# Kernel optimization log

Measured on AMD Instinct MI355X. Metric: run time of the kernel, lower is better.

Reference implementation:

```python
import jax, jax.numpy as jnp
import numpy as np

B, T, D = 2048, 60, 6
H, F, O = 64, 10, 1


def setup_inputs() -> dict:
    key = jax.random.key(0)
    ks = jax.random.split(key, 16)
    w = lambda k, shape, s=0.1: jax.random.normal(k, shape, jnp.float32) * s
    return {
        "x": jax.random.normal(ks[0], (B, T, D), jnp.float32),
        "W_i": w(ks[1], (D, H)), "U_i": w(ks[2], (H, H)), "b_i": jnp.zeros((H,), jnp.float32),
        "W_ste": w(ks[3], (D, H)), "U_ste": w(ks[4], (H, H)), "b_ste": jnp.ones((H,), jnp.float32),
        "W_fre": w(ks[5], (D, F)), "U_fre": w(ks[6], (H, F)), "b_fre": jnp.ones((F,), jnp.float32),
        "W_c": w(ks[7], (D, H)), "U_c": w(ks[8], (H, H)), "b_c": jnp.zeros((H,), jnp.float32),
        "W_o": w(ks[9], (D, H)), "U_o": w(ks[10], (H, H)), "b_o": jnp.zeros((H,), jnp.float32),
        "U_a": w(ks[11], (F, 1)), "b_a": jnp.zeros((H,), jnp.float32),
        "W_p": w(ks[12], (H, O)), "b_p": jnp.zeros((O,), jnp.float32),
    }


def _hsig(v):
    # torch.nn.Hardsigmoid: relu6(x + 3) / 6
    return jnp.clip(v / 6.0 + 0.5, 0.0, 1.0)


def reference(x, W_i, U_i, b_i, W_ste, U_ste, b_ste, W_fre, U_fre, b_fre,
              W_c, U_c, b_c, W_o, U_o, b_o, U_a, b_a, W_p, b_p):
    b, t_len, _ = x.shape
    h_dim = W_i.shape[1]
    f_dim = W_fre.shape[1]
    freq = jnp.arange(f_dim, dtype=x.dtype) / f_dim  # (F,)
    ua = U_a[:, 0]  # (F,)

    def step(carry, x_t):
        h, S_re, S_im, t = carry
        i = _hsig(x_t @ W_i + b_i + h @ U_i)              # (B,H)
        ste = _hsig(x_t @ W_ste + b_ste + h @ U_ste)      # (B,H)
        fre = _hsig(x_t @ W_fre + b_fre + h @ U_fre)      # (B,F)
        f = ste[:, :, None] * fre[:, None, :]             # (B,H,F)
        c = i * jnp.tanh(x_t @ W_c + b_c + h @ U_c)       # (B,H)
        t = t + 1.0
        omega = (2.0 * jnp.pi) * t * freq                  # (F,)
        S_re = f * S_re + c[:, :, None] * jnp.cos(omega)   # (B,H,F)
        S_im = f * S_im + c[:, :, None] * jnp.sin(omega)   # (B,H,F)
        A = S_re * S_re + S_im * S_im                      # (B,H,F)
        a = jnp.tanh(jnp.einsum('bhf,f->bh', A, ua) + b_a)
        o = _hsig(x_t @ W_o + b_o + h @ U_o)
        h = o * a
        return (h, S_re, S_im, t), None

    init = (jnp.zeros((b, h_dim), x.dtype),
            jnp.zeros((b, h_dim, f_dim), x.dtype),
            jnp.zeros((b, h_dim, f_dim), x.dtype),
            jnp.asarray(0.0, x.dtype))
    (h, _, _, _), _ = jax.lax.scan(step, init, jnp.swapaxes(x, 0, 1))
    # original returns p from the last timestep only
    return h @ W_p + b_p
```

## Files before the change

### kernel.cpp

```cpp
#include <hip/hip_runtime.h>


#define BB 2048
#define TT 60
#define DD 6
#define HH 64
#define FF 10
#define NB 4

#define XS 968
#define HS 72

typedef short bf16x8 __attribute__((ext_vector_type(8)));
typedef float f32x4  __attribute__((ext_vector_type(4)));

__device__ __forceinline__ unsigned short f2bf(float f) {
    union { float f; unsigned u; } v; v.f = f;
    unsigned r = v.u + 0x7fffu + ((v.u >> 16) & 1u);
    return (unsigned short)(r >> 16);
}
__device__ __forceinline__ float bf2f(unsigned short b) {
    union { unsigned u; float f; } v; v.u = ((unsigned)b) << 16; return v.f;
}
__device__ __forceinline__ float hsig_f(float v) {
    return fminf(fmaxf(fmaf(v, 0.16666666666666666f, 0.5f), 0.0f), 1.0f);
}
__device__ __forceinline__ float tanh_f(float x) {
    float xc = fminf(fmaxf(x, -12.0f), 12.0f);
    float e  = __builtin_amdgcn_exp2f(xc * 2.8853900817779268f);
    return (e - 1.0f) * __builtin_amdgcn_rcpf(e + 1.0f);
}
__device__ __forceinline__ float uni(float v) {
    return __int_as_float(__builtin_amdgcn_readfirstlane(__float_as_int(v)));
}
__device__ __forceinline__ void pinv(bf16x8& v) { asm volatile("" : "+v"(v)); }

__global__ __launch_bounds__(256, 2)
void sfm_kernel(
    const float* __restrict__ x,
    const float* __restrict__ W_i,  const float* __restrict__ U_i,  const float* __restrict__ b_i,
    const float* __restrict__ W_ste,const float* __restrict__ U_ste,const float* __restrict__ b_ste,
    const float* __restrict__ W_fre,const float* __restrict__ U_fre,const float* __restrict__ b_fre,
    const float* __restrict__ W_c,  const float* __restrict__ U_c,  const float* __restrict__ b_c,
    const float* __restrict__ W_o,  const float* __restrict__ U_o,  const float* __restrict__ b_o,
    const float* __restrict__ U_a,  const float* __restrict__ b_a,
    const float* __restrict__ W_p,  const float* __restrict__ b_p,
    float* __restrict__ out)
{
    const int tid  = threadIdx.x;
    const int lane = tid & 63;
    const int wave = tid >> 6;
    const int q    = lane >> 4;
    const int n16  = lane & 15;
    const int b0   = blockIdx.x * NB;

    __shared__ __align__(16) unsigned short xsp[NB * XS];
    __shared__ __align__(16) unsigned short hhi[NB * HS];
    __shared__ __align__(16) unsigned short hlo[NB * HS];
    __shared__ __align__(16) float zbuf[4 * 64 * NB];
    __shared__ __align__(16) float frebuf[16 * NB];
    __shared__ float red[4][NB];

    for (int item = tid; item < NB * TT; item += 256) {
        const float* xg = x + (size_t)b0 * (TT * DD) + item * DD;
        const int b = item / TT, s = item - b * TT;
        unsigned short* dst = &xsp[b * XS + s * 16];
        #pragma unroll
        for (int d = 0; d < DD; ++d) {
            const float v = xg[d];
            const unsigned short hb = f2bf(v);
            dst[d]     = hb;
            dst[8 + d] = f2bf(v - bf2f(hb));
        }
        dst[6] = 0x3F80; dst[7] = 0;
        dst[14] = 0; dst[15] = 0;
    }
    for (int i = tid; i < NB * HS; i += 256) { hhi[i] = 0; hlo[i] = 0; }

    const float* Ug = (wave == 0) ? U_i : (wave == 1) ? U_ste : (wave == 2) ? U_c : U_o;
    const float* Wg = (wave == 0) ? W_i : (wave == 1) ? W_ste : (wave == 2) ? W_c : W_o;
    const float* bg = (wave == 0) ? b_i : (wave == 1) ? b_ste : (wave == 2) ? b_c : b_o;

    bf16x8 Bh[5][3], Bl[5][3];
    #pragma unroll
    for (int t = 0; t < 5; ++t) {
        #pragma unroll
        for (int c = 0; c < 3; ++c) {
            #pragma unroll
            for (int j = 0; j < 8; ++j) {
                const int kv = c * 32 + q * 8 + j;
                float v = 0.0f;
                if (t < 4) {
                    const int n = t * 16 + n16;
                    if      (kv < 64)  v = Ug[kv * HH + n];
                    else if (kv < 70)  v = Wg[(kv - 64) * HH + n];
                    else if (kv == 70) v = bg[n];
                } else if (wave == 3 && n16 < FF) {
                    if      (kv < 64)  v = U_fre[kv * FF + n16];
                    else if (kv < 70)  v = W_fre[(kv - 64) * FF + n16];
                    else if (kv == 70) v = b_fre[n16];
                }
                const unsigned short hb = f2bf(v);
                Bh[t][c][j] = (short)hb;
                Bl[t][c][j] = (short)f2bf(v - bf2f(hb));
            }
            pinv(Bh[t][c]); pinv(Bl[t][c]);
        }
    }

    const int pb = tid & (NB - 1);
    const int pc = tid >> 2;
    const float bav = b_a[pc];
    const float wpv = W_p[pc];
    const float bpv = uni(b_p[0]);
    float uav[FF];
    #pragma unroll
    for (int f = 0; f < FF; ++f) uav[f] = uni(U_a[f]);

    const float CBt[FF] = { 1.0f,  0.8090169943749475f,  0.30901699437494745f,
                           -0.30901699437494745f, -0.8090169943749475f, -1.0f,
                           -0.8090169943749475f, -0.30901699437494745f,
                            0.30901699437494745f,  0.8090169943749475f };
    const float SBt[FF] = { 0.0f,  0.5877852522924731f,  0.9510565162951535f,
                            0.9510565162951535f,  0.5877852522924731f,  0.0f,
                           -0.5877852522924731f, -0.9510565162951535f,
                           -0.9510565162951535f, -0.5877852522924731f };

    float Sre[FF], Sim[FF], cs[FF], sn[FF];
    #pragma unroll
    for (int f = 0; f < FF; ++f) {
        Sre[f] = 0.0f; Sim[f] = 0.0f; cs[f] = CBt[f]; sn[f] = SBt[f];
    }
    float hv = 0.0f;

    __syncthreads();

    int sm = 0;
    for (int s = 0; s < TT; ++s) {
        const int ab = n16 & (NB - 1);
        bf16x8 Ah[3], Al[3];
        #pragma unroll
        for (int c = 0; c < 2; ++c) {
            Ah[c] = *(const bf16x8*)&hhi[ab * HS + c * 32 + q * 8];
            Al[c] = *(const bf16x8*)&hlo[ab * HS + c * 32 + q * 8];
        }
        {
            const bf16x8 xvh = *(const bf16x8*)&xsp[ab * XS + s * 16];
            const bf16x8 xvl = *(const bf16x8*)&xsp[ab * XS + s * 16 + 8];
            const bf16x8 zf = {0, 0, 0, 0, 0, 0, 0, 0};
            Ah[2] = (q == 0) ? xvh : zf;
            Al[2] = (q == 0) ? xvl : zf;
        }

        f32x4 acc[5];
        #pragma unroll
        for (int t = 0; t < 5; ++t) {
            if (t < 4 || wave == 3) {
                f32x4 a = {0.0f, 0.0f, 0.0f, 0.0f};
                #pragma unroll
                for (int c = 0; c < 3; ++c) {
                    a = __builtin_amdgcn_mfma_f32_16x16x32_bf16(Al[c], Bh[t][c], a, 0, 0, 0);
                    a = __builtin_amdgcn_mfma_f32_16x16x32_bf16(Ah[c], Bl[t][c], a, 0, 0, 0);
                    a = __builtin_amdgcn_mfma_f32_16x16x32_bf16(Ah[c], Bh[t][c], a, 0, 0, 0);
                }
                acc[t] = a;
            }
        }

        if (q == 0) {
            #pragma unroll
            for (int t = 0; t < 4; ++t)
                *(f32x4*)&zbuf[(wave * 64 + t * 16 + n16) * NB] = acc[t];
            if (wave == 3 && n16 < FF)
                *(f32x4*)&frebuf[n16 * NB] = acc[4];
        }
        __syncthreads();

        const float zi = zbuf[(0 * 64 + pc) * NB + pb];
        const float zs = zbuf[(1 * 64 + pc) * NB + pb];
        const float zc = zbuf[(2 * 64 + pc) * NB + pb];
        const float zo = zbuf[(3 * 64 + pc) * NB + pb];
        float fr[FF];
        #pragma unroll
        for (int f = 0; f < FF; ++f) fr[f] = hsig_f(frebuf[f * NB + pb]);

        const float iv  = hsig_f(zi);
        const float stv = hsig_f(zs);
        const float ov  = hsig_f(zo);
        const float cv  = iv * tanh_f(zc);

        if (sm == 0) {
            #pragma unroll
            for (int f = 0; f < FF; ++f) { cs[f] = CBt[f]; sn[f] = SBt[f]; }
        }

        float aacc = bav;
        #pragma unroll
        for (int f = 0; f < FF; ++f) {
            const float fc = stv * fr[f];
            Sre[f] = fmaf(fc, Sre[f], cv * cs[f]);
            Sim[f] = fmaf(fc, Sim[f], cv * sn[f]);
            const float A = fmaf(Sim[f], Sim[f], Sre[f] * Sre[f]);
            aacc = fmaf(A, uav[f], aacc);
            const float cc = cs[f];
            cs[f] = fmaf(cc, CBt[f], -(sn[f] * SBt[f]));
            sn[f] = fmaf(cc, SBt[f],   sn[f] * CBt[f]);
        }
        hv = ov * tanh_f(aacc);

        {
            const unsigned short hb = f2bf(hv);
            hhi[pb * HS + pc] = hb;
            hlo[pb * HS + pc] = f2bf(hv - bf2f(hb));
        }
        if (++sm == 10) sm = 0;
        __syncthreads();
    }

    float val = hv * wpv;
    val += __shfl_xor(val, 4, 64);
    val += __shfl_xor(val, 8, 64);
    val += __shfl_xor(val, 16, 64);
    val += __shfl_xor(val, 32, 64);
    if (lane < NB) red[wave][lane] = val;
    __syncthreads();
    if (tid < NB)
        out[b0 + tid] = red[0][tid] + red[1][tid] + red[2][tid] + red[3][tid] + bpv;
}

extern "C" void kernel_launch(void* const* d_in, const int* in_sizes, int n_in,
                              void* d_out, int out_size, void* d_ws, size_t ws_size,
                              hipStream_t stream) {
    (void)in_sizes; (void)n_in; (void)d_ws; (void)ws_size; (void)out_size;
    const float* x     = (const float*)d_in[0];
    const float* W_i   = (const float*)d_in[1];
    const float* U_i   = (const float*)d_in[2];
    const float* b_i   = (const float*)d_in[3];
    const float* W_ste = (const float*)d_in[4];
    const float* U_ste = (const float*)d_in[5];
    const float* b_ste = (const float*)d_in[6];
    const float* W_fre = (const float*)d_in[7];
    const float* U_fre = (const float*)d_in[8];
    const float* b_fre = (const float*)d_in[9];
    const float* W_c   = (const float*)d_in[10];
    const float* U_c   = (const float*)d_in[11];
    const float* b_c   = (const float*)d_in[12];
    const float* W_o   = (const float*)d_in[13];
    const float* U_o   = (const float*)d_in[14];
    const float* b_o   = (const float*)d_in[15];
    const float* U_a   = (const float*)d_in[16];
    const float* b_a   = (const float*)d_in[17];
    const float* W_p   = (const float*)d_in[18];
    const float* b_p   = (const float*)d_in[19];

    sfm_kernel<<<BB / NB, 256, 0, stream>>>(
        x, W_i, U_i, b_i, W_ste, U_ste, b_ste, W_fre, U_fre, b_fre,
        W_c, U_c, b_c, W_o, U_o, b_o, U_a, b_a, W_p, b_p, (float*)d_out);
}
```

Measured before the change: 177.3 us.

## Unroll recurrence by period 10 to make twiddles compile-time constants and interleave MFMAs

The time loop is split into 6 outer iterations of 10 fully unrolled steps. Because omega has period 10, the cos/sin twiddle factors become compile-time constants indexed by (f*(k+1))%10, which removes the per-step rotation recurrence and the reset branch. The five MFMA accumulation chains are also interleaved so independent accumulators overlap instead of running serially, and hardsigmoid uses a single med3 instruction. The full unroll grows code size and may raise register pressure.

```diff
diff --git a/kernel.cpp b/kernel.cpp
--- a/kernel.cpp
+++ b/kernel.cpp
@@ -23,7 +23,7 @@
     union { unsigned u; float f; } v; v.u = ((unsigned)b) << 16; return v.f;
 }
 __device__ __forceinline__ float hsig_f(float v) {
-    return fminf(fmaxf(fmaf(v, 0.16666666666666666f, 0.5f), 0.0f), 1.0f);
+    return __builtin_amdgcn_fmed3f(fmaf(v, 0.16666666666666666f, 0.5f), 0.0f, 1.0f);
 }
 __device__ __forceinline__ float tanh_f(float x) {
     float xc = fminf(fmaxf(x, -12.0f), 12.0f);
@@ -117,104 +117,101 @@
     #pragma unroll
     for (int f = 0; f < FF; ++f) uav[f] = uni(U_a[f]);
 
-    const float CBt[FF] = { 1.0f,  0.8090169943749475f,  0.30901699437494745f,
-                           -0.30901699437494745f, -0.8090169943749475f, -1.0f,
-                           -0.8090169943749475f, -0.30901699437494745f,
-                            0.30901699437494745f,  0.8090169943749475f };
-    const float SBt[FF] = { 0.0f,  0.5877852522924731f,  0.9510565162951535f,
-                            0.9510565162951535f,  0.5877852522924731f,  0.0f,
-                           -0.5877852522924731f, -0.9510565162951535f,
-                           -0.9510565162951535f, -0.5877852522924731f };
-
-    float Sre[FF], Sim[FF], cs[FF], sn[FF];
+    const float CT[FF] = { 1.0f,  0.8090169943749475f,  0.30901699437494745f,
+                          -0.30901699437494745f, -0.8090169943749475f, -1.0f,
+                          -0.8090169943749475f, -0.30901699437494745f,
+                           0.30901699437494745f,  0.8090169943749475f };
+    const float ST[FF] = { 0.0f,  0.5877852522924731f,  0.9510565162951535f,
+                           0.9510565162951535f,  0.5877852522924731f,  0.0f,
+                          -0.5877852522924731f, -0.9510565162951535f,
+                          -0.9510565162951535f, -0.5877852522924731f };
+
+    float Sre[FF], Sim[FF];
     #pragma unroll
-    for (int f = 0; f < FF; ++f) {
-        Sre[f] = 0.0f; Sim[f] = 0.0f; cs[f] = CBt[f]; sn[f] = SBt[f];
-    }
+    for (int f = 0; f < FF; ++f) { Sre[f] = 0.0f; Sim[f] = 0.0f; }
     float hv = 0.0f;
 
+    const int ab = n16 & (NB - 1);
+    const unsigned short* hhp = &hhi[ab * HS];
+    const unsigned short* hlp = &hlo[ab * HS];
+
     __syncthreads();
 
-    int sm = 0;
-    for (int s = 0; s < TT; ++s) {
-        const int ab = n16 & (NB - 1);
-        bf16x8 Ah[3], Al[3];
+    for (int sQ = 0; sQ < 6; ++sQ) {
+        const unsigned short* xrow = &xsp[ab * XS + sQ * 160];
         #pragma unroll
-        for (int c = 0; c < 2; ++c) {
-            Ah[c] = *(const bf16x8*)&hhi[ab * HS + c * 32 + q * 8];
-            Al[c] = *(const bf16x8*)&hlo[ab * HS + c * 32 + q * 8];
+        for (int k = 0; k < 10; ++k) {
+            bf16x8 Ah[3], Al[3];
+            #pragma unroll
+            for (int c = 0; c < 2; ++c) {
+                Ah[c] = *(const bf16x8*)&hhp[c * 32 + q * 8];
+                Al[c] = *(const bf16x8*)&hlp[c * 32 + q * 8];
+            }
+            {
+                const bf16x8 xvh = *(const bf16x8*)&xrow[k * 16];
+                const bf16x8 xvl = *(const bf16x8*)&xrow[k * 16 + 8];
+                const bf16x8 zf = {0, 0, 0, 0, 0, 0, 0, 0};
+                Ah[2] = (q == 0) ? xvh : zf;
+                Al[2] = (q == 0) ? xvl : zf;
+            }
+
+            f32x4 acc0 = {0.f,0.f,0.f,0.f}, acc1 = acc0, acc2 = acc0, acc3 = acc0, acc4 = acc0;
+            #pragma unroll
+            for (int c = 0; c < 3; ++c) {
+                #pragma unroll
+                for (int tm = 0; tm < 3; ++tm) {
+                    const bf16x8 a = (tm == 0) ? Al[c] : Ah[c];
+                    acc0 = __builtin_amdgcn_mfma_f32_16x16x32_bf16(a, (tm==1) ? Bl[0][c] : Bh[0][c], acc0, 0, 0, 0);
+                    acc1 = __builtin_amdgcn_mfma_f32_16x16x32_bf16(a, (tm==1) ? Bl[1][c] : Bh[1][c], acc1, 0, 0, 0);
+                    acc2 = __builtin_amdgcn_mfma_f32_16x16x32_bf16(a, (tm==1) ? Bl[2][c] : Bh[2][c], acc2, 0, 0, 0);
+                    acc3 = __builtin_amdgcn_mfma_f32_16x16x32_bf16(a, (tm==1) ? Bl[3][c] : Bh[3][c], acc3, 0, 0, 0);
+                    if (wave == 3)
+                        acc4 = __builtin_amdgcn_mfma_f32_16x16x32_bf16(a, (tm==1) ? Bl[4][c] : Bh[4][c], acc4, 0, 0, 0);
+                }
+            }
+
+            if (q == 0) {
+                *(f32x4*)&zbuf[(wave * 64 +  0 + n16) * NB] = acc0;
+                *(f32x4*)&zbuf[(wave * 64 + 16 + n16) * NB] = acc1;
+                *(f32x4*)&zbuf[(wave * 64 + 32 + n16) * NB] = acc2;
+                *(f32x4*)&zbuf[(wave * 64 + 48 + n16) * NB] = acc3;
+                if (wave == 3 && n16 < FF)
+                    *(f32x4*)&frebuf[n16 * NB] = acc4;
+            }
+            __syncthreads();
+
+            const float zi = zbuf[(0 * 64 + pc) * NB + pb];
+            const float zs = zbuf[(1 * 64 + pc) * NB + pb];
+            const float zc = zbuf[(2 * 64 + pc) * NB + pb];
+            const float zo = zbuf[(3 * 64 + pc) * NB + pb];
+            float fr[FF];
+            #pragma unroll
+            for (int f = 0; f < FF; ++f) fr[f] = hsig_f(frebuf[f * NB + pb]);
+
+            const float iv  = hsig_f(zi);
+            const float stv = hsig_f(zs);
+            const float ov  = hsig_f(zo);
+            const float cv  = iv * tanh_f(zc);
+
+            float aacc = bav;
+            #pragma unroll
+            for (int f = 0; f < FF; ++f) {
+                const int idx = (f * ((k + 1) % 10)) % 10;
+                const float fc = stv * fr[f];
+                Sre[f] = fmaf(fc, Sre[f], cv * CT[idx]);
+                Sim[f] = fmaf(fc, Sim[f], cv * ST[idx]);
+                const float A = fmaf(Sim[f], Sim[f], Sre[f] * Sre[f]);
+                aacc = fmaf(A, uav[f], aacc);
+            }
+            hv = ov * tanh_f(aacc);
+
+            {
+                const unsigned short hb = f2bf(hv);
+                hhi[pb * HS + pc] = hb;
+                hlo[pb * HS + pc] = f2bf(hv - bf2f(hb));
+            }
+            __syncthreads();
         }
-        {
-            const bf16x8 xvh = *(const bf16x8*)&xsp[ab * XS + s * 16];
-            const bf16x8 xvl = *(const bf16x8*)&xsp[ab * XS + s * 16 + 8];
-            const bf16x8 zf = {0, 0, 0, 0, 0, 0, 0, 0};
-            Ah[2] = (q == 0) ? xvh : zf;
-            Al[2] = (q == 0) ? xvl : zf;
-        }
-
-        f32x4 acc[5];
-        #pragma unroll
-        for (int t = 0; t < 5; ++t) {
-            if (t < 4 || wave == 3) {
-                f32x4 a = {0.0f, 0.0f, 0.0f, 0.0f};
-                #pragma unroll
-                for (int c = 0; c < 3; ++c) {
-                    a = __builtin_amdgcn_mfma_f32_16x16x32_bf16(Al[c], Bh[t][c], a, 0, 0, 0);
-                    a = __builtin_amdgcn_mfma_f32_16x16x32_bf16(Ah[c], Bl[t][c], a, 0, 0, 0);
-                    a = __builtin_amdgcn_mfma_f32_16x16x32_bf16(Ah[c], Bh[t][c], a, 0, 0, 0);
-                }
-                acc[t] = a;
-            }
-        }
-
-        if (q == 0) {
-            #pragma unroll
-            for (int t = 0; t < 4; ++t)
-                *(f32x4*)&zbuf[(wave * 64 + t * 16 + n16) * NB] = acc[t];
-            if (wave == 3 && n16 < FF)
-                *(f32x4*)&frebuf[n16 * NB] = acc[4];
-        }
-        __syncthreads();
-
-        const float zi = zbuf[(0 * 64 + pc) * NB + pb];
-        const float zs = zbuf[(1 * 64 + pc) * NB + pb];
-        const float zc = zbuf[(2 * 64 + pc) * NB + pb];
-        const float zo = zbuf[(3 * 64 + pc) * NB + pb];
-        float fr[FF];
-        #pragma unroll
-        for (int f = 0; f < FF; ++f) fr[f] = hsig_f(frebuf[f * NB + pb]);
-
-        const float iv  = hsig_f(zi);
-        const float stv = hsig_f(zs);
-        const float ov  = hsig_f(zo);
-        const float cv  = iv * tanh_f(zc);
-
-        if (sm == 0) {
-            #pragma unroll
-            for (int f = 0; f < FF; ++f) { cs[f] = CBt[f]; sn[f] = SBt[f]; }
-        }
-
-        float aacc = bav;
-        #pragma unroll
-        for (int f = 0; f < FF; ++f) {
-            const float fc = stv * fr[f];
-            Sre[f] = fmaf(fc, Sre[f], cv * cs[f]);
-            Sim[f] = fmaf(fc, Sim[f], cv * sn[f]);
-            const float A = fmaf(Sim[f], Sim[f], Sre[f] * Sre[f]);
-            aacc = fmaf(A, uav[f], aacc);
-            const float cc = cs[f];
-            cs[f] = fmaf(cc, CBt[f], -(sn[f] * SBt[f]));
-            sn[f] = fmaf(cc, SBt[f],   sn[f] * CBt[f]);
-        }
-        hv = ov * tanh_f(aacc);
-
-        {
-            const unsigned short hb = f2bf(hv);
-            hhi[pb * HS + pc] = hb;
-            hlo[pb * HS + pc] = f2bf(hv - bf2f(hb));
-        }
-        if (++sm == 10) sm = 0;
-        __syncthreads();
     }
 
     float val = hv * wpv;
```

Result: faster. 166.8 us (-5.9%).

## Double batch per block and split gate columns across eight waves

Applied to the files above, without the earlier changes.

Each block now handles 8 batch rows with 512 threads. Each of the 8 waves computes half the columns of one gate (2 MFMA tiles instead of 4), and the frequency gate moves to wave 7. Batch rows now fill 8 of the 16 MFMA M rows, so less of each matrix op is wasted, and each wave has a shorter serial MFMA chain per step. The MFMA loop is also interleaved across accumulators for ILP, and hardsigmoid uses fmed3. The cost is half as many blocks and larger blocks that may limit occupancy.

```diff
diff --git a/kernel.cpp b/kernel.cpp
--- a/kernel.cpp
+++ b/kernel.cpp
@@ -6,7 +6,7 @@
 #define DD 6
 #define HH 64
 #define FF 10
-#define NB 4
+#define NB 8
 
 #define XS 968
 #define HS 72
@@ -23,7 +23,7 @@
     union { unsigned u; float f; } v; v.u = ((unsigned)b) << 16; return v.f;
 }
 __device__ __forceinline__ float hsig_f(float v) {
-    return fminf(fmaxf(fmaf(v, 0.16666666666666666f, 0.5f), 0.0f), 1.0f);
+    return __builtin_amdgcn_fmed3f(fmaf(v, 0.16666666666666666f, 0.5f), 0.0f, 1.0f);
 }
 __device__ __forceinline__ float tanh_f(float x) {
     float xc = fminf(fmaxf(x, -12.0f), 12.0f);
@@ -35,7 +35,7 @@
 }
 __device__ __forceinline__ void pinv(bf16x8& v) { asm volatile("" : "+v"(v)); }
 
-__global__ __launch_bounds__(256, 2)
+__global__ __launch_bounds__(512, 2)
 void sfm_kernel(
     const float* __restrict__ x,
     const float* __restrict__ W_i,  const float* __restrict__ U_i,  const float* __restrict__ b_i,
@@ -59,11 +59,11 @@
     __shared__ __align__(16) unsigned short hlo[NB * HS];
     __shared__ __align__(16) float zbuf[4 * 64 * NB];
     __shared__ __align__(16) float frebuf[16 * NB];
-    __shared__ float red[4][NB];
-
-    for (int item = tid; item < NB * TT; item += 256) {
-        const float* xg = x + (size_t)b0 * (TT * DD) + item * DD;
-        const int b = item / TT, s = item - b * TT;
+    __shared__ float red[8][NB];
+
+    if (tid < NB * TT) {
+        const float* xg = x + (size_t)b0 * (TT * DD) + tid * DD;
+        const int b = tid / TT, s = tid - b * TT;
         unsigned short* dst = &xsp[b * XS + s * 16];
         #pragma unroll
         for (int d = 0; d < DD; ++d) {
@@ -75,27 +75,29 @@
         dst[6] = 0x3F80; dst[7] = 0;
         dst[14] = 0; dst[15] = 0;
     }
-    for (int i = tid; i < NB * HS; i += 256) { hhi[i] = 0; hlo[i] = 0; }
-
-    const float* Ug = (wave == 0) ? U_i : (wave == 1) ? U_ste : (wave == 2) ? U_c : U_o;
-    const float* Wg = (wave == 0) ? W_i : (wave == 1) ? W_ste : (wave == 2) ? W_c : W_o;
-    const float* bg = (wave == 0) ? b_i : (wave == 1) ? b_ste : (wave == 2) ? b_c : b_o;
-
-    bf16x8 Bh[5][3], Bl[5][3];
+    for (int i = tid; i < NB * HS; i += 512) { hhi[i] = 0; hlo[i] = 0; }
+
+    const int g = wave >> 1;
+    const int colbase = (wave & 1) * 32;
+    const float* Ug = (g == 0) ? U_i : (g == 1) ? U_ste : (g == 2) ? U_c : U_o;
+    const float* Wg = (g == 0) ? W_i : (g == 1) ? W_ste : (g == 2) ? W_c : W_o;
+    const float* bg = (g == 0) ? b_i : (g == 1) ? b_ste : (g == 2) ? b_c : b_o;
+
+    bf16x8 Bh[3][3], Bl[3][3];
     #pragma unroll
-    for (int t = 0; t < 5; ++t) {
+    for (int t = 0; t < 3; ++t) {
         #pragma unroll
         for (int c = 0; c < 3; ++c) {
             #pragma unroll
             for (int j = 0; j < 8; ++j) {
                 const int kv = c * 32 + q * 8 + j;
                 float v = 0.0f;
-                if (t < 4) {
-                    const int n = t * 16 + n16;
+                if (t < 2) {
+                    const int n = colbase + t * 16 + n16;
                     if      (kv < 64)  v = Ug[kv * HH + n];
                     else if (kv < 70)  v = Wg[(kv - 64) * HH + n];
                     else if (kv == 70) v = bg[n];
-                } else if (wave == 3 && n16 < FF) {
+                } else if (wave == 7 && n16 < FF) {
                     if      (kv < 64)  v = U_fre[kv * FF + n16];
                     else if (kv < 70)  v = W_fre[(kv - 64) * FF + n16];
                     else if (kv == 70) v = b_fre[n16];
@@ -109,7 +111,7 @@
     }
 
     const int pb = tid & (NB - 1);
-    const int pc = tid >> 2;
+    const int pc = tid >> 3;
     const float bav = b_a[pc];
     const float wpv = W_p[pc];
     const float bpv = uni(b_p[0]);
@@ -133,46 +135,48 @@
     }
     float hv = 0.0f;
 
+    const int ab = n16 & (NB - 1);
+    const unsigned short* hhp = &hhi[ab * HS];
+    const unsigned short* hlp = &hlo[ab * HS];
+    const unsigned short* xrow = &xsp[ab * XS];
+
     __syncthreads();
 
     int sm = 0;
     for (int s = 0; s < TT; ++s) {
-        const int ab = n16 & (NB - 1);
         bf16x8 Ah[3], Al[3];
         #pragma unroll
         for (int c = 0; c < 2; ++c) {
-            Ah[c] = *(const bf16x8*)&hhi[ab * HS + c * 32 + q * 8];
-            Al[c] = *(const bf16x8*)&hlo[ab * HS + c * 32 + q * 8];
+            Ah[c] = *(const bf16x8*)&hhp[c * 32 + q * 8];
+            Al[c] = *(const bf16x8*)&hlp[c * 32 + q * 8];
         }
         {
-            const bf16x8 xvh = *(const bf16x8*)&xsp[ab * XS + s * 16];
-            const bf16x8 xvl = *(const bf16x8*)&xsp[ab * XS + s * 16 + 8];
+            const bf16x8 xvh = *(const bf16x8*)&xrow[s * 16];
+            const bf16x8 xvl = *(const bf16x8*)&xrow[s * 16 + 8];
             const bf16x8 zf = {0, 0, 0, 0, 0, 0, 0, 0};
             Ah[2] = (q == 0) ? xvh : zf;
             Al[2] = (q == 0) ? xvl : zf;
         }
 
-        f32x4 acc[5];
-        #pragma unroll
-        for (int t = 0; t < 5; ++t) {
-            if (t < 4 || wave == 3) {
-                f32x4 a = {0.0f, 0.0f, 0.0f, 0.0f};
-                #pragma unroll
-                for (int c = 0; c < 3; ++c) {
-                    a = __builtin_amdgcn_mfma_f32_16x16x32_bf16(Al[c], Bh[t][c], a, 0, 0, 0);
-                    a = __builtin_amdgcn_mfma_f32_16x16x32_bf16(Ah[c], Bl[t][c], a, 0, 0, 0);
-                    a = __builtin_amdgcn_mfma_f32_16x16x32_bf16(Ah[c], Bh[t][c], a, 0, 0, 0);
-                }
-                acc[t] = a;
+        f32x4 acc0 = {0.f,0.f,0.f,0.f}, acc1 = acc0, acc2 = acc0;
+        #pragma unroll
+        for (int c = 0; c < 3; ++c) {
+            #pragma unroll
+            for (int tm = 0; tm < 3; ++tm) {
+                const bf16x8 a = (tm == 0) ? Al[c] : Ah[c];
+                acc0 = __builtin_amdgcn_mfma_f32_16x16x32_bf16(a, (tm==1) ? Bl[0][c] : Bh[0][c], acc0, 0, 0, 0);
+                acc1 = __builtin_amdgcn_mfma_f32_16x16x32_bf16(a, (tm==1) ? Bl[1][c] : Bh[1][c], acc1, 0, 0, 0);
+                if (wave == 7)
+                    acc2 = __builtin_amdgcn_mfma_f32_16x16x32_bf16(a, (tm==1) ? Bl[2][c] : Bh[2][c], acc2, 0, 0, 0);
             }
         }
 
-        if (q == 0) {
-            #pragma unroll
-            for (int t = 0; t < 4; ++t)
-                *(f32x4*)&zbuf[(wave * 64 + t * 16 + n16) * NB] = acc[t];
-            if (wave == 3 && n16 < FF)
-                *(f32x4*)&frebuf[n16 * NB] = acc[4];
+        if (q < 2) {
+            const int base = (g * 64 + colbase + n16) * NB + q * 4;
+            *(f32x4*)&zbuf[base]          = acc0;
+            *(f32x4*)&zbuf[base + 16*NB]  = acc1;
+            if (wave == 7)
+                *(f32x4*)&frebuf[n16 * NB + q * 4] = acc2;
         }
         __syncthreads();
 
@@ -218,14 +222,17 @@
     }
 
     float val = hv * wpv;
-    val += __shfl_xor(val, 4, 64);
     val += __shfl_xor(val, 8, 64);
     val += __shfl_xor(val, 16, 64);
     val += __shfl_xor(val, 32, 64);
     if (lane < NB) red[wave][lane] = val;
     __syncthreads();
-    if (tid < NB)
-        out[b0 + tid] = red[0][tid] + red[1][tid] + red[2][tid] + red[3][tid] + bpv;
+    if (tid < NB) {
+        float acc = bpv;
+        #pragma unroll
+        for (int w = 0; w < 8; ++w) acc += red[w][tid];
+        out[b0 + tid] = acc;
+    }
 }
 
 extern "C" void kernel_launch(void* const* d_in, const int* in_sizes, int n_in,
@@ -253,7 +260,7 @@
     const float* W_p   = (const float*)d_in[18];
     const float* b_p   = (const float*)d_in[19];
 
-    sfm_kernel<<<BB / NB, 256, 0, stream>>>(
+    sfm_kernel<<<BB / NB, 512, 0, stream>>>(
         x, W_i, U_i, b_i, W_ste, U_ste, b_ste, W_fre, U_fre, b_fre,
         W_c, U_c, b_c, W_o, U_o, b_o, U_a, b_a, W_p, b_p, (float*)d_out);
 }
```

Measured after the change: 163.7 us. 1.08x faster.

## Move input projections out of MFMA path and use trig lookup table

Applied to the files above, without the earlier changes.

Drops the third K-chunk (x, bias) from the per-step MFMA chain. The x@W projections are now computed in fp32 on the scalar/vector path per element, and the frequency-gate input projection is precomputed for all timesteps. The fre gate is packed into wave 3's fourth tile while wave 0 takes U_o's last tile, which balances MFMA work across waves (5/4/4/4 instead of 4/4/4/5). The cos/sin recurrence is replaced by a shared-memory lookup table indexed by timestep mod 10, and hardsigmoid uses med3. The cost is extra LDS reads and per-thread FMAs in the serial element-wise phase.

```diff
diff --git a/kernel.cpp b/kernel.cpp
--- a/kernel.cpp
+++ b/kernel.cpp
@@ -8,8 +8,8 @@
 #define FF 10
 #define NB 4
 
-#define XS 968
 #define HS 72
+#define XCS 964
 
 typedef short bf16x8 __attribute__((ext_vector_type(8)));
 typedef float f32x4  __attribute__((ext_vector_type(4)));
@@ -23,7 +23,7 @@
     union { unsigned u; float f; } v; v.u = ((unsigned)b) << 16; return v.f;
 }
 __device__ __forceinline__ float hsig_f(float v) {
-    return fminf(fmaxf(fmaf(v, 0.16666666666666666f, 0.5f), 0.0f), 1.0f);
+    return __builtin_amdgcn_fmed3f(fmaf(v, 0.16666666666666666f, 0.5f), 0.0f, 1.0f);
 }
 __device__ __forceinline__ float tanh_f(float x) {
     float xc = fminf(fmaxf(x, -12.0f), 12.0f);
@@ -54,52 +54,75 @@
     const int n16  = lane & 15;
     const int b0   = blockIdx.x * NB;
 
-    __shared__ __align__(16) unsigned short xsp[NB * XS];
+    __shared__ __align__(16) float xc[NB * XCS];
     __shared__ __align__(16) unsigned short hhi[NB * HS];
     __shared__ __align__(16) unsigned short hlo[NB * HS];
     __shared__ __align__(16) float zbuf[4 * 64 * NB];
-    __shared__ __align__(16) float frebuf[16 * NB];
+    __shared__ __align__(16) float frebuf[NB * 12];
+    __shared__ __align__(16) float ctab[10 * 10 * 2];
+    __shared__ float cstabB[10 * 2];
     __shared__ float red[4][NB];
 
-    for (int item = tid; item < NB * TT; item += 256) {
-        const float* xg = x + (size_t)b0 * (TT * DD) + item * DD;
-        const int b = item / TT, s = item - b * TT;
-        unsigned short* dst = &xsp[b * XS + s * 16];
-        #pragma unroll
-        for (int d = 0; d < DD; ++d) {
-            const float v = xg[d];
-            const unsigned short hb = f2bf(v);
-            dst[d]     = hb;
-            dst[8 + d] = f2bf(v - bf2f(hb));
-        }
-        dst[6] = 0x3F80; dst[7] = 0;
-        dst[14] = 0; dst[15] = 0;
+    for (int i = tid; i < NB * TT * DD; i += 256) {
+        const int b = i / (TT * DD), rem = i - b * (TT * DD);
+        const int s = rem / DD, d = rem - s * DD;
+        xc[b * XCS + s * 16 + d] = x[(size_t)b0 * (TT * DD) + i];
+    }
+    if (tid < 10) {
+        const float CTc[10] = { 1.0f,  0.8090169943749475f,  0.30901699437494745f,
+                               -0.30901699437494745f, -0.8090169943749475f, -1.0f,
+                               -0.8090169943749475f, -0.30901699437494745f,
+                                0.30901699437494745f,  0.8090169943749475f };
+        const float STc[10] = { 0.0f,  0.5877852522924731f,  0.9510565162951535f,
+                                0.9510565162951535f,  0.5877852522924731f,  0.0f,
+                               -0.5877852522924731f, -0.9510565162951535f,
+                               -0.9510565162951535f, -0.5877852522924731f };
+        float cc = 0.0f, ss = 0.0f;
+        #pragma unroll
+        for (int j = 0; j < 10; ++j) if (tid == j) { cc = CTc[j]; ss = STc[j]; }
+        cstabB[tid * 2] = cc; cstabB[tid * 2 + 1] = ss;
     }
     for (int i = tid; i < NB * HS; i += 256) { hhi[i] = 0; hlo[i] = 0; }
-
-    const float* Ug = (wave == 0) ? U_i : (wave == 1) ? U_ste : (wave == 2) ? U_c : U_o;
-    const float* Wg = (wave == 0) ? W_i : (wave == 1) ? W_ste : (wave == 2) ? W_c : W_o;
-    const float* bg = (wave == 0) ? b_i : (wave == 1) ? b_ste : (wave == 2) ? b_c : b_o;
-
-    bf16x8 Bh[5][3], Bl[5][3];
+    __syncthreads();
+
+    if (tid < NB * TT) {
+        const int b = tid / TT, s = tid - b * TT;
+        float xr[DD];
+        #pragma unroll
+        for (int d = 0; d < DD; ++d) xr[d] = xc[b * XCS + s * 16 + d];
+        #pragma unroll
+        for (int f = 0; f < FF; ++f) {
+            float v = b_fre[f];
+            #pragma unroll
+            for (int d = 0; d < DD; ++d) v = fmaf(xr[d], W_fre[d * FF + f], v);
+            xc[b * XCS + s * 16 + 6 + f] = v;
+        }
+    }
+    if (tid < 100) {
+        const int mm = tid / 10, ff = tid - mm * 10;
+        const int idx = (ff * mm) % 10;
+        ctab[tid * 2]     = cstabB[idx * 2];
+        ctab[tid * 2 + 1] = cstabB[idx * 2 + 1];
+    }
+
+    const int NT = (wave == 0) ? 5 : 4;
+    bf16x8 Bh[5][2], Bl[5][2];
     #pragma unroll
     for (int t = 0; t < 5; ++t) {
-        #pragma unroll
-        for (int c = 0; c < 3; ++c) {
+        if (t >= NT) continue;
+        const bool isfre = (t == 3 && wave == 3);
+        const int g  = (t == 4) ? 3 : wave;
+        const int cb = (t == 3 || t == 4) ? 48 : t * 16;
+        const float* Up = isfre ? U_fre :
+                          (g == 0) ? U_i : (g == 1) ? U_ste : (g == 2) ? U_c : U_o;
+        #pragma unroll
+        for (int c = 0; c < 2; ++c) {
             #pragma unroll
             for (int j = 0; j < 8; ++j) {
                 const int kv = c * 32 + q * 8 + j;
-                float v = 0.0f;
-                if (t < 4) {
-                    const int n = t * 16 + n16;
-                    if      (kv < 64)  v = Ug[kv * HH + n];
-                    else if (kv < 70)  v = Wg[(kv - 64) * HH + n];
-                    else if (kv == 70) v = bg[n];
-                } else if (wave == 3 && n16 < FF) {
-                    if      (kv < 64)  v = U_fre[kv * FF + n16];
-                    else if (kv < 70)  v = W_fre[(kv - 64) * FF + n16];
-                    else if (kv == 70) v = b_fre[n16];
-                }
+                float v;
+                if (isfre) v = (n16 < FF) ? Up[kv * FF + n16] : 0.0f;
+                else       v = Up[kv * HH + cb + n16];
                 const unsigned short hb = f2bf(v);
                 Bh[t][c][j] = (short)hb;
                 Bl[t][c][j] = (short)f2bf(v - bf2f(hb));
@@ -116,95 +139,108 @@
     float uav[FF];
     #pragma unroll
     for (int f = 0; f < FF; ++f) uav[f] = uni(U_a[f]);
-
-    const float CBt[FF] = { 1.0f,  0.8090169943749475f,  0.30901699437494745f,
-                           -0.30901699437494745f, -0.8090169943749475f, -1.0f,
-                           -0.8090169943749475f, -0.30901699437494745f,
-                            0.30901699437494745f,  0.8090169943749475f };
-    const float SBt[FF] = { 0.0f,  0.5877852522924731f,  0.9510565162951535f,
-                            0.9510565162951535f,  0.5877852522924731f,  0.0f,
-                           -0.5877852522924731f, -0.9510565162951535f,
-                           -0.9510565162951535f, -0.5877852522924731f };
-
-    float Sre[FF], Sim[FF], cs[FF], sn[FF];
-    #pragma unroll
-    for (int f = 0; f < FF; ++f) {
-        Sre[f] = 0.0f; Sim[f] = 0.0f; cs[f] = CBt[f]; sn[f] = SBt[f];
-    }
+    float wxi[DD], wxs[DD], wxc[DD], wxo[DD];
+    #pragma unroll
+    for (int d = 0; d < DD; ++d) {
+        wxi[d] = W_i[d * HH + pc];  wxs[d] = W_ste[d * HH + pc];
+        wxc[d] = W_c[d * HH + pc];  wxo[d] = W_o[d * HH + pc];
+    }
+    const float bi = b_i[pc], bs = b_ste[pc], bc = b_c[pc], bo = b_o[pc];
+
+    float Sre[FF], Sim[FF];
+    #pragma unroll
+    for (int f = 0; f < FF; ++f) { Sre[f] = 0.0f; Sim[f] = 0.0f; }
     float hv = 0.0f;
 
+    const int ab = n16 & (NB - 1);
+    const unsigned short* hhp = &hhi[ab * HS];
+    const unsigned short* hlp = &hlo[ab * HS];
+
     __syncthreads();
 
-    int sm = 0;
+    int m = 1;
     for (int s = 0; s < TT; ++s) {
-        const int ab = n16 & (NB - 1);
-        bf16x8 Ah[3], Al[3];
+        bf16x8 Ah[2], Al[2];
         #pragma unroll
         for (int c = 0; c < 2; ++c) {
-            Ah[c] = *(const bf16x8*)&hhi[ab * HS + c * 32 + q * 8];
-            Al[c] = *(const bf16x8*)&hlo[ab * HS + c * 32 + q * 8];
-        }
-        {
-            const bf16x8 xvh = *(const bf16x8*)&xsp[ab * XS + s * 16];
-            const bf16x8 xvl = *(const bf16x8*)&xsp[ab * XS + s * 16 + 8];
-            const bf16x8 zf = {0, 0, 0, 0, 0, 0, 0, 0};
-            Ah[2] = (q == 0) ? xvh : zf;
-            Al[2] = (q == 0) ? xvl : zf;
+            Ah[c] = *(const bf16x8*)&hhp[c * 32 + q * 8];
+            Al[c] = *(const bf16x8*)&hlp[c * 32 + q * 8];
         }
 
         f32x4 acc[5];
         #pragma unroll
         for (int t = 0; t < 5; ++t) {
-            if (t < 4 || wave == 3) {
-                f32x4 a = {0.0f, 0.0f, 0.0f, 0.0f};
-                #pragma unroll
-                for (int c = 0; c < 3; ++c) {
-                    a = __builtin_amdgcn_mfma_f32_16x16x32_bf16(Al[c], Bh[t][c], a, 0, 0, 0);
-                    a = __builtin_amdgcn_mfma_f32_16x16x32_bf16(Ah[c], Bl[t][c], a, 0, 0, 0);
-                    a = __builtin_amdgcn_mfma_f32_16x16x32_bf16(Ah[c], Bh[t][c], a, 0, 0, 0);
+            if (t >= NT) continue;
+            f32x4 a = {0.0f, 0.0f, 0.0f, 0.0f};
+            #pragma unroll
+            for (int c = 0; c < 2; ++c) {
+                a = __builtin_amdgcn_mfma_f32_16x16x32_bf16(Al[c], Bh[t][c], a, 0, 0, 0);
+                a = __builtin_amdgcn_mfma_f32_16x16x32_bf16(Ah[c], Bl[t][c], a, 0, 0, 0);
+                a = __builtin_amdgcn_mfma_f32_16x16x32_bf16(Ah[c], Bh[t][c], a, 0, 0, 0);
+            }
+            acc[t] = a;
+        }
+
+        if (q == 0) {
+            *(f32x4*)&zbuf[(wave * 64 +  0 + n16) * NB] = acc[0];
+            *(f32x4*)&zbuf[(wave * 64 + 16 + n16) * NB] = acc[1];
+            *(f32x4*)&zbuf[(wave * 64 + 32 + n16) * NB] = acc[2];
+            if (wave == 3) {
+                if (n16 < FF) {
+                    #pragma unroll
+                    for (int r = 0; r < 4; ++r)
+                        frebuf[r * 12 + n16] = acc[3][r] + xc[r * XCS + s * 16 + 6 + n16];
                 }
-                acc[t] = a;
+            } else {
+                *(f32x4*)&zbuf[(wave * 64 + 48 + n16) * NB] = acc[3];
             }
-        }
-
-        if (q == 0) {
-            #pragma unroll
-            for (int t = 0; t < 4; ++t)
-                *(f32x4*)&zbuf[(wave * 64 + t * 16 + n16) * NB] = acc[t];
-            if (wave == 3 && n16 < FF)
-                *(f32x4*)&frebuf[n16 * NB] = acc[4];
+            if (wave == 0)
+                *(f32x4*)&zbuf[(3 * 64 + 48 + n16) * NB] = acc[4];
         }
         __syncthreads();
 
-        const float zi = zbuf[(0 * 64 + pc) * NB + pb];
-        const float zs = zbuf[(1 * 64 + pc) * NB + pb];
-        const float zc = zbuf[(2 * 64 + pc) * NB + pb];
-        const float zo = zbuf[(3 * 64 + pc) * NB + pb];
+        const float4 xv4 = *(const float4*)&xc[pb * XCS + s * 16];
+        const float2 xv2 = *(const float2*)&xc[pb * XCS + s * 16 + 4];
+        const float xa[DD] = {xv4.x, xv4.y, xv4.z, xv4.w, xv2.x, xv2.y};
+
+        float vi = bi, vs = bs, vc = bc, vo = bo;
+        #pragma unroll
+        for (int d = 0; d < DD; ++d) {
+            vi = fmaf(xa[d], wxi[d], vi);
+            vs = fmaf(xa[d], wxs[d], vs);
+            vc = fmaf(xa[d], wxc[d], vc);
+            vo = fmaf(xa[d], wxo[d], vo);
+        }
+        const float zi = zbuf[(0 * 64 + pc) * NB + pb] + vi;
+        const float zs = zbuf[(1 * 64 + pc) * NB + pb] + vs;
+        const float zc = zbuf[(2 * 64 + pc) * NB + pb] + vc;
+        const float zo = zbuf[(3 * 64 + pc) * NB + pb] + vo;
+
+        const f32x4 fb0 = *(const f32x4*)&frebuf[pb * 12];
+        const f32x4 fb1 = *(const f32x4*)&frebuf[pb * 12 + 4];
+        const f32x4 fb2 = *(const f32x4*)&frebuf[pb * 12 + 8];
         float fr[FF];
         #pragma unroll
-        for (int f = 0; f < FF; ++f) fr[f] = hsig_f(frebuf[f * NB + pb]);
+        for (int f = 0; f < 4; ++f) fr[f] = hsig_f(fb0[f]);
+        #pragma unroll
+        for (int f = 0; f < 4; ++f) fr[4 + f] = hsig_f(fb1[f]);
+        fr[8] = hsig_f(fb2[0]); fr[9] = hsig_f(fb2[1]);
 
         const float iv  = hsig_f(zi);
         const float stv = hsig_f(zs);
         const float ov  = hsig_f(zo);
         const float cv  = iv * tanh_f(zc);
 
-        if (sm == 0) {
-            #pragma unroll
-            for (int f = 0; f < FF; ++f) { cs[f] = CBt[f]; sn[f] = SBt[f]; }
-        }
-
+        const float* tp = &ctab[m * 20];
         float aacc = bav;
         #pragma unroll
         for (int f = 0; f < FF; ++f) {
+            const float2 tv = *(const float2*)&tp[f * 2];
             const float fc = stv * fr[f];
-            Sre[f] = fmaf(fc, Sre[f], cv * cs[f]);
-            Sim[f] = fmaf(fc, Sim[f], cv * sn[f]);
+            Sre[f] = fmaf(fc, Sre[f], cv * tv.x);
+            Sim[f] = fmaf(fc, Sim[f], cv * tv.y);
             const float A = fmaf(Sim[f], Sim[f], Sre[f] * Sre[f]);
             aacc = fmaf(A, uav[f], aacc);
-            const float cc = cs[f];
-            cs[f] = fmaf(cc, CBt[f], -(sn[f] * SBt[f]));
-            sn[f] = fmaf(cc, SBt[f],   sn[f] * CBt[f]);
         }
         hv = ov * tanh_f(aacc);
 
@@ -213,7 +249,7 @@
             hhi[pb * HS + pc] = hb;
             hlo[pb * HS + pc] = f2bf(hv - bf2f(hb));
         }
-        if (++sm == 10) sm = 0;
+        if (++m == 10) m = 0;
         __syncthreads();
     }
 
```

Result: faster. 159.1 us (-10.3%).
